# Optimization experiments

Hardware: AMD Instinct MI355X
Metric: run time of the kernel (lower is better)

## Reference

```python
import jax, jax.numpy as jnp
import numpy as np

N_NODES = 100000
N_EDGES = 3200000  # avg degree 32
D_IN = 256
D_OUT = 256


def setup_inputs() -> dict:
    key = jax.random.key(0)
    k1, k2, k3, k4 = jax.random.split(key, 4)
    x = jax.random.normal(k1, (N_NODES, D_IN), dtype=jnp.float32)
    # nn.Linear(in, out, bias=False): weight shape [out, in]
    W = jax.random.normal(k2, (D_OUT, D_IN), dtype=jnp.float32) / np.sqrt(D_IN).astype(np.float32)
    bias = jnp.zeros((D_OUT,), dtype=jnp.float32)
    rows = jax.random.randint(k3, (N_EDGES,), 0, N_NODES, dtype=jnp.int32)
    cols = jax.random.randint(k4, (N_EDGES,), 0, N_NODES, dtype=jnp.int32)
    return {"x": x, "W": W, "bias": bias, "rows": rows, "cols": cols}


def reference(x, W, bias, rows, cols):
    # aggr == 'planetoid-gcn-residual' branch; dropout p=0 (identity).
    n = x.shape[0]
    h = x @ W.T + bias                                      # [N, D_out]
    # adj_t.sum(dim=-1): per-row degree of binary adjacency
    deg = jax.ops.segment_sum(jnp.ones(rows.shape, x.dtype), rows, num_segments=n)
    norm = jax.lax.rsqrt(1.0 + deg)[:, None]                # [N, 1]
    h = norm * h
    # spmm_add(adj_t, h)[i] = sum_{(i,j) in E} h[j]
    agg = jax.ops.segment_sum(h[cols], rows, num_segments=n)
    h = agg + h
    return norm * h
```

## Files before the change

### kernel.cpp

```cpp
#include <hip/hip_runtime.h>
#include <hip/hip_fp16.h>
#include <stdint.h>


#define THREADS 256
#define NB 512
#define B3_EDGES 8192

typedef _Float16 half8 __attribute__((ext_vector_type(8)));
typedef float floatx4 __attribute__((ext_vector_type(4)));

__global__ __launch_bounds__(THREADS) void bucket_count(
    const int* __restrict__ rows, int* __restrict__ bcnt, int E, int nbuck) {
    __shared__ int h[NB];
    h[threadIdx.x] = 0; h[threadIdx.x + 256] = 0;
    __syncthreads();
    int nquad  = E >> 2;
    int stride = gridDim.x * THREADS;
    for (int q = blockIdx.x * THREADS + threadIdx.x; q < nquad; q += stride) {
        int4 r = ((const int4*)rows)[q];
        atomicAdd(&h[r.x >> 8], 1);
        atomicAdd(&h[r.y >> 8], 1);
        atomicAdd(&h[r.z >> 8], 1);
        atomicAdd(&h[r.w >> 8], 1);
    }
    if (blockIdx.x == 0)
        for (int e = (nquad << 2) + threadIdx.x; e < E; e += THREADS)
            atomicAdd(&h[rows[e] >> 8], 1);
    __syncthreads();
    for (int b = threadIdx.x; b < nbuck; b += THREADS) {
        int v = h[b];
        if (v) atomicAdd(&bcnt[b], v);
    }
}

__global__ __launch_bounds__(THREADS) void bucket_scan(
    const int* __restrict__ bcnt, int* __restrict__ boff, int* __restrict__ bcur,
    int nbuck, int E) {
    __shared__ int s1[THREADS];
    int tid = threadIdx.x;
    int b0 = 2 * tid, b1 = 2 * tid + 1;
    int v0 = (b0 < nbuck) ? bcnt[b0] : 0;
    int v1 = (b1 < nbuck) ? bcnt[b1] : 0;
    s1[tid] = v0 + v1;
    __syncthreads();
    for (int off = 1; off < THREADS; off <<= 1) {
        int t = (tid >= off) ? s1[tid - off] : 0;
        __syncthreads();
        s1[tid] += t;
        __syncthreads();
    }
    int excl = s1[tid] - (v0 + v1);
    if (b0 < nbuck) { boff[b0] = excl;      bcur[b0] = excl; }
    if (b1 < nbuck) { boff[b1] = excl + v0; bcur[b1] = excl + v0; }
    if (tid == 0) boff[nbuck] = E;
}

__global__ __launch_bounds__(THREADS) void bucket_scatter(
    const int* __restrict__ rows, const int* __restrict__ cols,
    int* __restrict__ bcur, uint32_t* __restrict__ buf, int E, int nbuck) {
    __shared__ uint32_t staged[B3_EDGES];
    __shared__ int h[NB], lo[NB], gb[NB], hc[NB], s1[THREADS];
    int tid = threadIdx.x;
    h[tid] = 0; h[tid + 256] = 0;
    __syncthreads();
    int e0 = blockIdx.x * B3_EDGES;
    int e1 = e0 + B3_EDGES; if (e1 > E) e1 = E;
    for (int e = e0 + tid; e < e1; e += THREADS)
        atomicAdd(&h[rows[e] >> 8], 1);
    __syncthreads();
    int a0 = h[2 * tid], a1 = h[2 * tid + 1];
    s1[tid] = a0 + a1;
    __syncthreads();
    for (int off = 1; off < THREADS; off <<= 1) {
        int t = (tid >= off) ? s1[tid - off] : 0;
        __syncthreads();
        s1[tid] += t;
        __syncthreads();
    }
    int eps = s1[tid] - (a0 + a1);
    lo[2 * tid]     = eps;
    lo[2 * tid + 1] = eps + a0;
    for (int b = tid; b < NB; b += THREADS) {
        int v = h[b];
        gb[b] = (b < nbuck && v) ? atomicAdd(&bcur[b], v) : 0;
        hc[b] = 0;
    }
    __syncthreads();
    for (int e = e0 + tid; e < e1; e += THREADS) {
        int r = rows[e];
        int c = cols[e];
        int b = r >> 8;
        int p = lo[b] + atomicAdd(&hc[b], 1);
        staged[p] = ((uint32_t)(r & 255) << 17) | (uint32_t)c;
    }
    __syncthreads();
    int wid = tid >> 6, lane = tid & 63;
    for (int b = wid; b < nbuck; b += 4) {
        int cnt = h[b], src = lo[b], dst = gb[b];
        for (int i = lane; i < cnt; i += 64)
            buf[dst + i] = staged[src + i];
    }
}

__global__ __launch_bounds__(THREADS) void csr_finalize(
    const uint32_t* __restrict__ buf, const int* __restrict__ boff,
    int* __restrict__ rs, int* __restrict__ csr, int n, int E) {
    int b   = blockIdx.x;
    int tid = threadIdx.x;
    __shared__ int h[256], base[256], s1[THREADS];
    h[tid] = 0;
    __syncthreads();
    int s = boff[b], e = boff[b + 1];
    for (int i = s + tid; i < e; i += THREADS)
        atomicAdd(&h[buf[i] >> 17], 1);
    __syncthreads();
    int v = h[tid];
    s1[tid] = v;
    __syncthreads();
    for (int off = 1; off < THREADS; off <<= 1) {
        int t = (tid >= off) ? s1[tid - off] : 0;
        __syncthreads();
        s1[tid] += t;
        __syncthreads();
    }
    int myBase = s + s1[tid] - v;
    base[tid] = myBase;
    int row = (b << 8) + tid;
    if (row < n) rs[row] = myBase;
    h[tid] = 0;
    if (b == 0 && tid == 0) rs[n] = E;
    __syncthreads();
    for (int i = s + tid; i < e; i += THREADS) {
        uint32_t p = buf[i];
        int rl = p >> 17;
        int c  = p & 0x1FFFF;
        int q  = base[rl] + atomicAdd(&h[rl], 1);
        csr[q] = c;
    }
}

__global__ void make_bswz(const float* __restrict__ W, half8* __restrict__ Bswz) {
    int t = blockIdx.x * THREADS + threadIdx.x;
    int n_tile = t >> 9;
    int k_step = (t >> 6) & 7;
    int lane   = t & 63;
    int q = lane >> 4, m16 = lane & 15;
    const float* src = W + (size_t)(n_tile * 16 + m16) * 256 + k_step * 32 + q * 8;
    half8 h;
#pragma unroll
    for (int j = 0; j < 8; j++) h[j] = (_Float16)src[j];
    Bswz[t] = h;
}

__global__ __launch_bounds__(THREADS) void gemm_mfma(
    const float* __restrict__ x, const half8* __restrict__ Bswz,
    const float* __restrict__ bias, const int* __restrict__ rs,
    _Float16* __restrict__ h16, int n) {
    __shared__ _Float16 As[4 * 8 * 64 * 8];
    int tid  = threadIdx.x;
    int row0 = blockIdx.x * 64;

#pragma unroll
    for (int i = 0; i < 8; i++) {
        int entry  = i * 256 + tid;
        int m_sub  = entry >> 9;
        int k_step = (entry >> 6) & 7;
        int lw     = entry & 63;
        int r      = m_sub * 16 + (lw & 15);
        int k      = k_step * 32 + (lw >> 4) * 8;
        float4 v0, v1;
        if (row0 + r < n) {
            const float* src = x + (size_t)(row0 + r) * 256 + k;
            v0 = *(const float4*)src;
            v1 = *(const float4*)(src + 4);
        } else {
            v0.x = v0.y = v0.z = v0.w = 0.f;
            v1.x = v1.y = v1.z = v1.w = 0.f;
        }
        union { _Float16 h[8]; uint4 u; } pk;
        pk.h[0] = (_Float16)v0.x; pk.h[1] = (_Float16)v0.y;
        pk.h[2] = (_Float16)v0.z; pk.h[3] = (_Float16)v0.w;
        pk.h[4] = (_Float16)v1.x; pk.h[5] = (_Float16)v1.y;
        pk.h[6] = (_Float16)v1.z; pk.h[7] = (_Float16)v1.w;
        *(uint4*)(As + entry * 8) = pk.u;
    }
    __syncthreads();

    int w    = tid >> 6;
    int lane = tid & 63;

    floatx4 acc[4][4];
#pragma unroll
    for (int ms = 0; ms < 4; ms++)
#pragma unroll
        for (int nn = 0; nn < 4; nn++) {
            acc[ms][nn][0] = 0.f; acc[ms][nn][1] = 0.f;
            acc[ms][nn][2] = 0.f; acc[ms][nn][3] = 0.f;
        }

    half8 bf[2][4], af[2][4];
#pragma unroll
    for (int nn = 0; nn < 4; nn++)
        bf[0][nn] = Bswz[((w * 4 + nn) * 8 + 0) * 64 + lane];
#pragma unroll
    for (int ms = 0; ms < 4; ms++)
        af[0][ms] = *(const half8*)(As + ((ms * 8 + 0) * 64 + lane) * 8);

#pragma unroll
    for (int ks = 0; ks < 8; ks++) {
        int cur = ks & 1, nxt = cur ^ 1;
        if (ks < 7) {
#pragma unroll
            for (int nn = 0; nn < 4; nn++)
                bf[nxt][nn] = Bswz[((w * 4 + nn) * 8 + ks + 1) * 64 + lane];
#pragma unroll
            for (int ms = 0; ms < 4; ms++)
                af[nxt][ms] = *(const half8*)(As + ((ms * 8 + ks + 1) * 64 + lane) * 8);
        }
#pragma unroll
        for (int ms = 0; ms < 4; ms++)
#pragma unroll
            for (int nn = 0; nn < 4; nn++)
                acc[ms][nn] = __builtin_amdgcn_mfma_f32_16x16x32_f16(
                    af[cur][ms], bf[cur][nn], acc[ms][nn], 0, 0, 0);
    }

    int rgrp = lane >> 4;
    int cl   = lane & 15;
#pragma unroll
    for (int ms = 0; ms < 4; ms++) {
        int rbase = row0 + ms * 16 + rgrp * 4;
        float nrm[4];
#pragma unroll
        for (int i = 0; i < 4; i++) {
            int r = rbase + i;
            nrm[i] = (r < n) ? rsqrtf(1.0f + (float)(rs[r + 1] - rs[r])) : 0.f;
        }
#pragma unroll
        for (int nn = 0; nn < 4; nn++) {
            int col = w * 64 + nn * 16 + cl;
            float bb = bias[col];
#pragma unroll
            for (int i = 0; i < 4; i++) {
                int r = rbase + i;
                if (r < n)
                    h16[(size_t)r * 256 + col] =
                        (_Float16)((acc[ms][nn][i] + bb) * nrm[i]);
            }
        }
    }
}

__global__ __launch_bounds__(THREADS) void agg_rows(
    const _Float16* __restrict__ h16, const int* __restrict__ csr_col,
    const int* __restrict__ rs, float* __restrict__ out, int r0, int r1) {
    int row = r0 + blockIdx.x * 4 + (threadIdx.x >> 6);
    if (row >= r1) return;
    int lane = threadIdx.x & 63;
    int half = lane >> 5;
    int l32  = lane & 31;
    int off  = l32 * 8;

    int s   = rs[row];
    int end = rs[row + 1];

    float acc[8] = {0.f, 0.f, 0.f, 0.f, 0.f, 0.f, 0.f, 0.f};
    if (half == 0) {
        half8 v = *(const half8*)(h16 + (size_t)row * 256 + off);
#pragma unroll
        for (int j = 0; j < 8; j++) acc[j] = (float)v[j];
    }

    int e = s + half;
    for (; e + 2 < end; e += 4) {
        int c0 = csr_col[e];
        int c1 = csr_col[e + 2];
        half8 v0 = *(const half8*)(h16 + (size_t)c0 * 256 + off);
        half8 v1 = *(const half8*)(h16 + (size_t)c1 * 256 + off);
#pragma unroll
        for (int j = 0; j < 8; j++) acc[j] += (float)v0[j] + (float)v1[j];
    }
    for (; e < end; e += 2) {
        int c = csr_col[e];
        half8 v = *(const half8*)(h16 + (size_t)c * 256 + off);
#pragma unroll
        for (int j = 0; j < 8; j++) acc[j] += (float)v[j];
    }

#pragma unroll
    for (int j = 0; j < 8; j++) acc[j] += __shfl_down(acc[j], 32);

    if (half == 0) {
        float nrm = rsqrtf(1.0f + (float)(end - s));
        floatx4 o0, o1;
        o0[0] = acc[0] * nrm; o0[1] = acc[1] * nrm; o0[2] = acc[2] * nrm; o0[3] = acc[3] * nrm;
        o1[0] = acc[4] * nrm; o1[1] = acc[5] * nrm; o1[2] = acc[6] * nrm; o1[3] = acc[7] * nrm;
        float* dst = out + (size_t)row * 256 + off;
        __builtin_nontemporal_store(o0, (floatx4*)dst);
        __builtin_nontemporal_store(o1, (floatx4*)(dst + 4));
    }
}

extern "C" void kernel_launch(void* const* d_in, const int* in_sizes, int n_in,
                              void* d_out, int out_size, void* d_ws, size_t ws_size,
                              hipStream_t stream) {
    const float* x    = (const float*)d_in[0];
    const float* W    = (const float*)d_in[1];
    const float* bias = (const float*)d_in[2];
    const int*   rows = (const int*)d_in[3];
    const int*   cols = (const int*)d_in[4];

    const int D = 256;
    int n = in_sizes[0] / D;
    int E = in_sizes[3];
    int nbuck = (n + 255) >> 8;

    char* p = (char*)d_ws;
    auto alignup = [](size_t v) { return (v + 255) & ~(size_t)255; };
    _Float16* h16 = (_Float16*)p; p += alignup((size_t)n * D * sizeof(_Float16));
    int*   rs     = (int*)p;    p += alignup((size_t)(n + 1) * sizeof(int));
    int*   csr    = (int*)p;    p += alignup((size_t)E * sizeof(int));
    half8* Bswz   = (half8*)p;  p += alignup((size_t)8192 * sizeof(half8));
    int*   bcnt   = (int*)p;    p += alignup((size_t)NB * sizeof(int));
    int*   boff   = (int*)p;    p += alignup((size_t)(NB + 1) * sizeof(int));
    int*   bcur   = (int*)p;    p += alignup((size_t)NB * sizeof(int));

    uint32_t* buf = (uint32_t*)h16;

    hipMemsetAsync(bcnt, 0, (size_t)nbuck * sizeof(int), stream);

    bucket_count<<<256, THREADS, 0, stream>>>(rows, bcnt, E, nbuck);
    bucket_scan<<<1, THREADS, 0, stream>>>(bcnt, boff, bcur, nbuck, E);

    int b3blocks = (E + B3_EDGES - 1) / B3_EDGES;
    bucket_scatter<<<b3blocks, THREADS, 0, stream>>>(rows, cols, bcur, buf, E, nbuck);

    csr_finalize<<<nbuck, THREADS, 0, stream>>>(buf, boff, rs, csr, n, E);

    make_bswz<<<32, THREADS, 0, stream>>>(W, Bswz);

    int gblocks = (n + 63) / 64;
    gemm_mfma<<<gblocks, THREADS, 0, stream>>>(x, Bswz, bias, rs, h16, n);

    int half_n = (n + 1) / 2;
    int ab0 = (half_n + 3) / 4;
    int ab1 = ((n - half_n) + 3) / 4;
    agg_rows<<<ab0, THREADS, 0, stream>>>(h16, csr, rs, (float*)d_out, 0, half_n);
    agg_rows<<<ab1, THREADS, 0, stream>>>(h16, csr, rs, (float*)d_out, half_n, n);
}
```

Measured before the change: 548.2 us.

## Split aggregation into column quarters, stage CSR buckets in LDS, fuse weight swizzle

New measurement: 551.3 us. About the same (+0.6%).

```diff
diff --git a/kernel.cpp b/kernel.cpp
--- a/kernel.cpp
+++ b/kernel.cpp
@@ -6,17 +6,33 @@
 #define THREADS 256
 #define NB 512
 #define B3_EDGES 8192
+#define B5_CAP 10240
+#define COUNT_BLOCKS 256
 
 typedef _Float16 half8 __attribute__((ext_vector_type(8)));
 typedef float floatx4 __attribute__((ext_vector_type(4)));
 
-__global__ __launch_bounds__(THREADS) void bucket_count(
-    const int* __restrict__ rows, int* __restrict__ bcnt, int E, int nbuck) {
+__global__ __launch_bounds__(THREADS) void bucket_count_bswz(
+    const int* __restrict__ rows, int* __restrict__ bcnt,
+    const float* __restrict__ W, half8* __restrict__ Bswz, int E, int nbuck) {
+    if (blockIdx.x >= COUNT_BLOCKS) {
+        int t = (blockIdx.x - COUNT_BLOCKS) * THREADS + threadIdx.x;
+        int n_tile = t >> 9;
+        int k_step = (t >> 6) & 7;
+        int lane   = t & 63;
+        int q = lane >> 4, m16 = lane & 15;
+        const float* src = W + (size_t)(n_tile * 16 + m16) * 256 + k_step * 32 + q * 8;
+        half8 h;
+#pragma unroll
+        for (int j = 0; j < 8; j++) h[j] = (_Float16)src[j];
+        Bswz[t] = h;
+        return;
+    }
     __shared__ int h[NB];
     h[threadIdx.x] = 0; h[threadIdx.x + 256] = 0;
     __syncthreads();
     int nquad  = E >> 2;
-    int stride = gridDim.x * THREADS;
+    int stride = COUNT_BLOCKS * THREADS;
     for (int q = blockIdx.x * THREADS + threadIdx.x; q < nquad; q += stride) {
         int4 r = ((const int4*)rows)[q];
         atomicAdd(&h[r.x >> 8], 1);
@@ -108,12 +124,23 @@
     int* __restrict__ rs, int* __restrict__ csr, int n, int E) {
     int b   = blockIdx.x;
     int tid = threadIdx.x;
+    __shared__ uint32_t sbuf[B5_CAP];
     __shared__ int h[256], base[256], s1[THREADS];
     h[tid] = 0;
     __syncthreads();
     int s = boff[b], e = boff[b + 1];
-    for (int i = s + tid; i < e; i += THREADS)
-        atomicAdd(&h[buf[i] >> 17], 1);
+    int cnt = e - s;
+    bool fit = (cnt <= B5_CAP);
+    if (fit) {
+        for (int i = tid; i < cnt; i += THREADS) {
+            uint32_t v = buf[s + i];
+            sbuf[i] = v;
+            atomicAdd(&h[v >> 17], 1);
+        }
+    } else {
+        for (int i = s + tid; i < e; i += THREADS)
+            atomicAdd(&h[buf[i] >> 17], 1);
+    }
     __syncthreads();
     int v = h[tid];
     s1[tid] = v;
@@ -131,26 +158,21 @@
     h[tid] = 0;
     if (b == 0 && tid == 0) rs[n] = E;
     __syncthreads();
-    for (int i = s + tid; i < e; i += THREADS) {
-        uint32_t p = buf[i];
-        int rl = p >> 17;
-        int c  = p & 0x1FFFF;
-        int q  = base[rl] + atomicAdd(&h[rl], 1);
-        csr[q] = c;
-    }
-}
-
-__global__ void make_bswz(const float* __restrict__ W, half8* __restrict__ Bswz) {
-    int t = blockIdx.x * THREADS + threadIdx.x;
-    int n_tile = t >> 9;
-    int k_step = (t >> 6) & 7;
-    int lane   = t & 63;
-    int q = lane >> 4, m16 = lane & 15;
-    const float* src = W + (size_t)(n_tile * 16 + m16) * 256 + k_step * 32 + q * 8;
-    half8 h;
-#pragma unroll
-    for (int j = 0; j < 8; j++) h[j] = (_Float16)src[j];
-    Bswz[t] = h;
+    if (fit) {
+        for (int i = tid; i < cnt; i += THREADS) {
+            uint32_t p = sbuf[i];
+            int rl = p >> 17;
+            int q  = base[rl] + atomicAdd(&h[rl], 1);
+            csr[q] = (int)(p & 0x1FFFF);
+        }
+    } else {
+        for (int i = s + tid; i < e; i += THREADS) {
+            uint32_t p = buf[i];
+            int rl = p >> 17;
+            int q  = base[rl] + atomicAdd(&h[rl], 1);
+            csr[q] = (int)(p & 0x1FFFF);
+        }
+    }
 }
 
 __global__ __launch_bounds__(THREADS) void gemm_mfma(
@@ -252,46 +274,51 @@
     }
 }
 
-__global__ __launch_bounds__(THREADS) void agg_rows(
+__global__ __launch_bounds__(THREADS) void agg_q(
     const _Float16* __restrict__ h16, const int* __restrict__ csr_col,
-    const int* __restrict__ rs, float* __restrict__ out, int r0, int r1) {
-    int row = r0 + blockIdx.x * 4 + (threadIdx.x >> 6);
-    if (row >= r1) return;
+    const int* __restrict__ rs, float* __restrict__ out, int n, int qsel) {
+    int row = blockIdx.x * 4 + (threadIdx.x >> 6);
+    if (row >= n) return;
     int lane = threadIdx.x & 63;
-    int half = lane >> 5;
-    int l32  = lane & 31;
-    int off  = l32 * 8;
+    int g    = lane >> 3;
+    int l8   = lane & 7;
+    int off  = qsel * 64 + l8 * 8;
+    const _Float16* hb = h16 + off;
 
     int s   = rs[row];
     int end = rs[row + 1];
 
     float acc[8] = {0.f, 0.f, 0.f, 0.f, 0.f, 0.f, 0.f, 0.f};
-    if (half == 0) {
-        half8 v = *(const half8*)(h16 + (size_t)row * 256 + off);
+    if (g == 0) {
+        half8 v = *(const half8*)(hb + (size_t)row * 256);
 #pragma unroll
         for (int j = 0; j < 8; j++) acc[j] = (float)v[j];
     }
 
-    int e = s + half;
-    for (; e + 2 < end; e += 4) {
+    int e = s + g;
+    for (; e + 8 < end; e += 16) {
         int c0 = csr_col[e];
-        int c1 = csr_col[e + 2];
-        half8 v0 = *(const half8*)(h16 + (size_t)c0 * 256 + off);
-        half8 v1 = *(const half8*)(h16 + (size_t)c1 * 256 + off);
+        int c1 = csr_col[e + 8];
+        half8 v0 = *(const half8*)(hb + (size_t)c0 * 256);
+        half8 v1 = *(const half8*)(hb + (size_t)c1 * 256);
 #pragma unroll
         for (int j = 0; j < 8; j++) acc[j] += (float)v0[j] + (float)v1[j];
     }
-    for (; e < end; e += 2) {
+    for (; e < end; e += 8) {
         int c = csr_col[e];
-        half8 v = *(const half8*)(h16 + (size_t)c * 256 + off);
+        half8 v = *(const half8*)(hb + (size_t)c * 256);
 #pragma unroll
         for (int j = 0; j < 8; j++) acc[j] += (float)v[j];
     }
 
 #pragma unroll
     for (int j = 0; j < 8; j++) acc[j] += __shfl_down(acc[j], 32);
-
-    if (half == 0) {
+#pragma unroll
+    for (int j = 0; j < 8; j++) acc[j] += __shfl_down(acc[j], 16);
+#pragma unroll
+    for (int j = 0; j < 8; j++) acc[j] += __shfl_down(acc[j], 8);
+
+    if (g == 0) {
         float nrm = rsqrtf(1.0f + (float)(end - s));
         floatx4 o0, o1;
         o0[0] = acc[0] * nrm; o0[1] = acc[1] * nrm; o0[2] = acc[2] * nrm; o0[3] = acc[3] * nrm;
@@ -330,7 +357,8 @@
 
     hipMemsetAsync(bcnt, 0, (size_t)nbuck * sizeof(int), stream);
 
-    bucket_count<<<256, THREADS, 0, stream>>>(rows, bcnt, E, nbuck);
+    bucket_count_bswz<<<COUNT_BLOCKS + 32, THREADS, 0, stream>>>(
+        rows, bcnt, W, Bswz, E, nbuck);
     bucket_scan<<<1, THREADS, 0, stream>>>(bcnt, boff, bcur, nbuck, E);
 
     int b3blocks = (E + B3_EDGES - 1) / B3_EDGES;
@@ -338,14 +366,12 @@
 
     csr_finalize<<<nbuck, THREADS, 0, stream>>>(buf, boff, rs, csr, n, E);
 
-    make_bswz<<<32, THREADS, 0, stream>>>(W, Bswz);
-
     int gblocks = (n + 63) / 64;
     gemm_mfma<<<gblocks, THREADS, 0, stream>>>(x, Bswz, bias, rs, h16, n);
 
-    int half_n = (n + 1) / 2;
-    int ab0 = (half_n + 3) / 4;
-    int ab1 = ((n - half_n) + 3) / 4;
-    agg_rows<<<ab0, THREADS, 0, stream>>>(h16, csr, rs, (float*)d_out, 0, half_n);
-    agg_rows<<<ab1, THREADS, 0, stream>>>(h16, csr, rs, (float*)d_out, half_n, n);
-}
+    int ablocks = (n + 3) / 4;
+    agg_q<<<ablocks, THREADS, 0, stream>>>(h16, csr, rs, (float*)d_out, n, 0);
+    agg_q<<<ablocks, THREADS, 0, stream>>>(h16, csr, rs, (float*)d_out, n, 1);
+    agg_q<<<ablocks, THREADS, 0, stream>>>(h16, csr, rs, (float*)d_out, n, 2);
+    agg_q<<<ablocks, THREADS, 0, stream>>>(h16, csr, rs, (float*)d_out, n, 3);
+}
```
